# Kernel tuning notes

Hardware: AMD Instinct MI355X
Metric: run time of the kernel (lower is better)

## Reference

```python
import jax, jax.numpy as jnp
import numpy as np

B, S, M = 8, 2048, 256
D = 512          # input/memory feature dim
P = 512          # proj_dim
H = 8            # num_heads


def setup_inputs() -> dict:
    key = jax.random.key(0)
    ks = jax.random.split(key, 10)
    sc = 0.02
    return {
        "input_seq": jax.random.normal(ks[0], (B, S, D), jnp.float32),
        "memory_cells": jax.random.normal(ks[1], (B, M, D), jnp.float32),
        "Wk": jax.random.normal(ks[2], (D, P), jnp.float32) * sc,
        "bk": jnp.zeros((P,), jnp.float32),
        "Wv": jax.random.normal(ks[3], (D, P), jnp.float32) * sc,
        "bv": jnp.zeros((P,), jnp.float32),
        "Wq": jax.random.normal(ks[4], (H, D, P), jnp.float32) * sc,  # stacked per-head query Dense
        "bq": jnp.zeros((H, P), jnp.float32),
        "Wo": jax.random.normal(ks[5], (H * P, P), jnp.float32) * sc,
        "bo": jnp.zeros((P,), jnp.float32),
    }


def reference(input_seq, memory_cells, Wk, bk, Wv, bv, Wq, bq, Wo, bo):
    # shared key/value projections (multi-query: one K/V for all heads)
    ik = input_seq @ Wk + bk          # [B,S,P]
    mk = memory_cells @ Wk + bk       # [B,M,P]
    iv = input_seq @ Wv + bv          # [B,S,P]
    mv = memory_cells @ Wv + bv       # [B,M,P]

    # per-head queries from memory cells, all heads at once
    q = jnp.einsum('bmd,hdp->bhmp', memory_cells, Wq) + bq[None, :, None, :]  # [B,H,M,P]

    input_score = jnp.einsum('bhmp,bsp->bhms', q, ik)          # [B,H,M,S]
    self_score = jnp.sum(q * mk[:, None], axis=-1, keepdims=True)  # [B,H,M,1]
    score = jnp.concatenate([self_score, input_score], axis=-1)    # [B,H,M,S+1]
    score = score / jnp.sqrt(jnp.float32(P))
    attn = jax.nn.softmax(score, axis=-1)

    self_attn = attn[..., 0:1]                                  # [B,H,M,1]
    input_attn = attn[..., 1:]                                  # [B,H,M,S]
    val = jnp.einsum('bhms,bsp->bhmp', input_attn, iv) + self_attn * mv[:, None]

    # concat heads: [B,M,H*P]
    concat = jnp.transpose(val, (0, 2, 1, 3)).reshape(B, M, H * P)
    return concat @ Wo + bo           # [B,M,P]
```

## Files before the change

### kernel.cpp

```cpp
#include <hip/hip_runtime.h>

#define B_ 8
#define S_ 2048
#define M_ 256
#define D_ 512
#define P_ 512
#define H_ 8

#define SCALE 0.044194173824159216f

typedef __attribute__((ext_vector_type(8))) short bf16x8;
typedef __attribute__((ext_vector_type(4))) float f32x4;

static __device__ __forceinline__ float bf2f(short u) {
  union { float f; unsigned int i; } x;
  x.i = ((unsigned int)(unsigned short)u) << 16;
  return x.f;
}
static __device__ __forceinline__ short f2bf(float f) {
  union { float f; unsigned int i; } x;
  x.f = f;
  unsigned int r = (x.i + 0x7FFFu + ((x.i >> 16) & 1u)) >> 16;
  return (short)r;
}

static __device__ __forceinline__ void gll16(const short* g, short* l) {
  __builtin_amdgcn_global_load_lds(
      (const __attribute__((address_space(1))) void*)g,
      (__attribute__((address_space(3))) void*)l, 16, 0, 0);
}

#define LGKM_WAIT() asm volatile("s_waitcnt lgkmcnt(0)" ::: "memory")

__global__ __launch_bounds__(256) void cast_both(
    const float* __restrict__ inA, short* __restrict__ outA, int n4A,
    const float* __restrict__ inM, short* __restrict__ outM)
{
  int idx = blockIdx.x * 256 + threadIdx.x;
  const float* in = inA;
  short* out = outA;
  if (idx >= n4A) { idx -= n4A; in = inM; out = outM; }
  float4 v = ((const float4*)in)[idx];
  short o0 = f2bf(v.x), o1 = f2bf(v.y), o2 = f2bf(v.z), o3 = f2bf(v.w);
  uint2 pk;
  pk.x = (unsigned int)(unsigned short)o0 | ((unsigned int)(unsigned short)o1 << 16);
  pk.y = (unsigned int)(unsigned short)o2 | ((unsigned int)(unsigned short)o3 << 16);
  ((uint2*)out)[idx] = pk;
}

__global__ __launch_bounds__(256) void wtrans_g(
    const float* __restrict__ in, short* __restrict__ out, int kdim, int ndim)
{
  __shared__ float tile[32][33];
  const int t = threadIdx.x, tx = t & 31, ty = t >> 5;
  const size_t zofs = (size_t)blockIdx.z * kdim * ndim;
  const int n0 = blockIdx.x * 32, k0 = blockIdx.y * 32;
  const float* inp = in + zofs;
  short* outp = out + zofs;
#pragma unroll
  for (int i = 0; i < 4; ++i)
    tile[ty + 8 * i][tx] = inp[(size_t)(k0 + ty + 8 * i) * ndim + n0 + tx];
  __syncthreads();
#pragma unroll
  for (int i = 0; i < 4; ++i)
    outp[(size_t)(n0 + ty + 8 * i) * kdim + k0 + tx] = f2bf(tile[tx][ty + 8 * i]);
}

__global__ __launch_bounds__(256) void zero_f(float* __restrict__ p) {
  ((float4*)p)[blockIdx.x * 256 + threadIdx.x] = make_float4(0.f, 0.f, 0.f, 0.f);
}

template<int MODE, int K, int N, int LDA, int LDB>
__global__ __launch_bounds__(256) void gemm128(
    const short* __restrict__ Abase, const short* __restrict__ Bbase,
    const float* __restrict__ bias, void* __restrict__ Cv,
    const size_t aZ, const int bzsh, const size_t bZ, const size_t cZ,
    float* __restrict__ Ls,
    const float* __restrict__ eselfp, const short* __restrict__ mvbp)
{
  __shared__ short As[8192];
  __shared__ short Bs[8192];
  const int t = threadIdx.x;
  const int w = t >> 6, lane = t & 63, qd = lane >> 4, ln = lane & 15;
  const int z = blockIdx.z;
  const int n0 = blockIdx.x * 128, m0 = blockIdx.y * 128;
  const int wm = (w & 1) * 64, wn = (w >> 1) * 64;

  const short* A  = Abase + (size_t)z * aZ;
  const short* Bp = Bbase + (size_t)(z >> bzsh) * bZ;

  const int rr = t >> 3, gph = t & 7;
  const int gl = gph ^ ((rr >> 1) & 7);
  const short* gaT = A + (size_t)(m0 + rr) * LDA + gl * 8;
  const short* gbT = Bp + (size_t)(n0 + rr) * LDB + gl * 8;

  int aoff[4], boff[4];
#pragma unroll
  for (int mt = 0; mt < 4; ++mt) {
    int r = wm + mt * 16 + ln;
    aoff[mt] = r * 64 + (qd ^ ((r >> 1) & 7)) * 8;
  }
#pragma unroll
  for (int nt = 0; nt < 4; ++nt) {
    int r = wn + nt * 16 + ln;
    boff[nt] = r * 64 + (qd ^ ((r >> 1) & 7)) * 8;
  }

  f32x4 acc[4][4];
#pragma unroll
  for (int mt = 0; mt < 4; ++mt)
#pragma unroll
    for (int nt = 0; nt < 4; ++nt) acc[mt][nt] = (f32x4){0.f, 0.f, 0.f, 0.f};

  for (int kc = 0; kc < K; kc += 64) {
    __syncthreads();
#pragma unroll
    for (int c = 0; c < 4; ++c) {
      gll16(gaT + (size_t)c * 32 * LDA + kc, &As[c * 2048 + w * 512]);
      gll16(gbT + (size_t)c * 32 * LDB + kc, &Bs[c * 2048 + w * 512]);
    }
    __syncthreads();
#pragma unroll
    for (int ch = 0; ch < 2; ++ch) {
      const int x = ch * 32;
      bf16x8 af[4], bfr[4];
#pragma unroll
      for (int mt = 0; mt < 4; ++mt) af[mt] = *(const bf16x8*)&As[aoff[mt] ^ x];
#pragma unroll
      for (int nt = 0; nt < 4; ++nt) bfr[nt] = *(const bf16x8*)&Bs[boff[nt] ^ x];
#pragma unroll
      for (int mt = 0; mt < 4; ++mt)
#pragma unroll
        for (int nt = 0; nt < 4; ++nt)
          acc[mt][nt] = __builtin_amdgcn_mfma_f32_16x16x32_bf16(af[mt], bfr[nt], acc[mt][nt], 0, 0, 0);
    }
  }

  if constexpr (MODE == 5) {
#pragma unroll
    for (int nt = 0; nt < 4; ++nt) {
      const int col = n0 + wn + nt * 16 + ln;
#pragma unroll
      for (int mt = 0; mt < 4; ++mt)
#pragma unroll
        for (int r = 0; r < 4; ++r) {
          const int row = m0 + wm + mt * 16 + qd * 4 + r;
          ((float*)Cv)[(size_t)z * cZ + (size_t)row * N + col] = acc[mt][nt][r];
        }
    }
  } else if constexpr (MODE == 2) {
#pragma unroll
    for (int mt = 0; mt < 4; ++mt)
#pragma unroll
      for (int nt = 0; nt < 4; ++nt)
#pragma unroll
        for (int r = 0; r < 4; ++r)
          acc[mt][nt][r] = __expf(acc[mt][nt][r] * SCALE);
#pragma unroll
    for (int mt = 0; mt < 4; ++mt)
#pragma unroll
      for (int r = 0; r < 4; ++r) {
        float rsum = acc[mt][0][r] + acc[mt][1][r] + acc[mt][2][r] + acc[mt][3][r];
        rsum += __shfl_xor(rsum, 1);
        rsum += __shfl_xor(rsum, 2);
        rsum += __shfl_xor(rsum, 4);
        rsum += __shfl_xor(rsum, 8);
        if (ln == 0) {
          const int row = m0 + wm + mt * 16 + qd * 4 + r;
          atomicAdd(&Ls[(size_t)z * M_ + row], rsum);
        }
      }
#pragma unroll
    for (int nt = 0; nt < 4; ++nt) {
      const int col = n0 + wn + nt * 16 + ln;
#pragma unroll
      for (int mt = 0; mt < 4; ++mt)
#pragma unroll
        for (int r = 0; r < 4; ++r) {
          const int row = m0 + wm + mt * 16 + qd * 4 + r;
          ((short*)Cv)[(size_t)z * cZ + (size_t)row * N + col] = f2bf(acc[mt][nt][r]);
        }
    }
  } else if constexpr (MODE == 3) {
    const int zb = z >> 3, hh = z & 7;
#pragma unroll
    for (int mt = 0; mt < 4; ++mt)
#pragma unroll
      for (int r = 0; r < 4; ++r) {
        const int row = m0 + wm + mt * 16 + qd * 4 + r;
        const float es = eselfp[(size_t)z * M_ + row];
        const float inv = 1.f / (es + Ls[(size_t)z * M_ + row]);
        const short* mvr = mvbp + ((size_t)(zb * M_ + row)) * P_;
        short* outr = (short*)Cv + ((size_t)(zb * M_ + row)) * (H_ * P_) + (size_t)hh * P_;
#pragma unroll
        for (int nt = 0; nt < 4; ++nt) {
          const int col = n0 + wn + nt * 16 + ln;
          outr[col] = f2bf((acc[mt][nt][r] + es * bf2f(mvr[col])) * inv);
        }
      }
  } else {
#pragma unroll
    for (int nt = 0; nt < 4; ++nt) {
      const int col = n0 + wn + nt * 16 + ln;
      const float bc = bias[512 * z + col];
#pragma unroll
      for (int mt = 0; mt < 4; ++mt)
#pragma unroll
        for (int r = 0; r < 4; ++r) {
          const int row = m0 + wm + mt * 16 + qd * 4 + r;
          const int bidx = row >> 8, ml = row & 255;
          ((short*)Cv)[((size_t)(bidx * H_ + z) * M_ + ml) * N + col] = f2bf(acc[mt][nt][r] + bc);
        }
    }
  }
}

template<bool TRANSV>
__global__ __launch_bounds__(256) void proj_kv(
    const short* __restrict__ A,
    const short* __restrict__ WkT, const short* __restrict__ WvT,
    const float* __restrict__ bk, const float* __restrict__ bv,
    short* __restrict__ Ck, short* __restrict__ Cvv)
{
  __shared__ short As[8192];
  __shared__ short Bks[4096];
  __shared__ short Bvs[4096];
  const int t = threadIdx.x;
  const int w = t >> 6, lane = t & 63, qd = lane >> 4, ln = lane & 15;
  const int n0 = blockIdx.x * 64, m0 = blockIdx.y * 128;
  const int wm = (w & 1) * 64, wn2 = (w >> 1) * 32;

  const int rr = t >> 3, gph = t & 7;
  const int gl = gph ^ ((rr >> 1) & 7);
  const short* gaT = A + (size_t)(m0 + rr) * 512 + gl * 8;
  const short* gbkT = WkT + (size_t)(n0 + rr) * 512 + gl * 8;
  const short* gbvT = WvT + (size_t)(n0 + rr) * 512 + gl * 8;

  int aoff[4], boff[2];
#pragma unroll
  for (int mt = 0; mt < 4; ++mt) {
    int r = wm + mt * 16 + ln;
    aoff[mt] = r * 64 + (qd ^ ((r >> 1) & 7)) * 8;
  }
#pragma unroll
  for (int nt = 0; nt < 2; ++nt) {
    int r = wn2 + nt * 16 + ln;
    boff[nt] = r * 64 + (qd ^ ((r >> 1) & 7)) * 8;
  }

  f32x4 accK[4][2], accV[4][2];
#pragma unroll
  for (int mt = 0; mt < 4; ++mt)
#pragma unroll
    for (int nt = 0; nt < 2; ++nt) {
      accK[mt][nt] = (f32x4){0.f, 0.f, 0.f, 0.f};
      accV[mt][nt] = (f32x4){0.f, 0.f, 0.f, 0.f};
    }

  for (int kc = 0; kc < 512; kc += 64) {
    __syncthreads();
#pragma unroll
    for (int c = 0; c < 4; ++c)
      gll16(gaT + (size_t)c * 32 * 512 + kc, &As[c * 2048 + w * 512]);
#pragma unroll
    for (int c = 0; c < 2; ++c) {
      gll16(gbkT + (size_t)c * 32 * 512 + kc, &Bks[c * 2048 + w * 512]);
      gll16(gbvT + (size_t)c * 32 * 512 + kc, &Bvs[c * 2048 + w * 512]);
    }
    __syncthreads();
#pragma unroll
    for (int ch = 0; ch < 2; ++ch) {
      const int x = ch * 32;
      bf16x8 af[4], bkf[2], bvf[2];
#pragma unroll
      for (int mt = 0; mt < 4; ++mt) af[mt] = *(const bf16x8*)&As[aoff[mt] ^ x];
#pragma unroll
      for (int nt = 0; nt < 2; ++nt) {
        bkf[nt] = *(const bf16x8*)&Bks[boff[nt] ^ x];
        bvf[nt] = *(const bf16x8*)&Bvs[boff[nt] ^ x];
      }
#pragma unroll
      for (int mt = 0; mt < 4; ++mt)
#pragma unroll
        for (int nt = 0; nt < 2; ++nt) {
          accK[mt][nt] = __builtin_amdgcn_mfma_f32_16x16x32_bf16(af[mt], bkf[nt], accK[mt][nt], 0, 0, 0);
          accV[mt][nt] = __builtin_amdgcn_mfma_f32_16x16x32_bf16(af[mt], bvf[nt], accV[mt][nt], 0, 0, 0);
        }
    }
  }

#pragma unroll
  for (int nt = 0; nt < 2; ++nt) {
    const int col = n0 + wn2 + nt * 16 + ln;
    const float bc = bk[col];
#pragma unroll
    for (int mt = 0; mt < 4; ++mt)
#pragma unroll
      for (int r = 0; r < 4; ++r) {
        const int row = m0 + wm + mt * 16 + qd * 4 + r;
        Ck[(size_t)row * 512 + col] = f2bf(accK[mt][nt][r] + bc);
      }
  }

  if constexpr (!TRANSV) {
#pragma unroll
    for (int nt = 0; nt < 2; ++nt) {
      const int col = n0 + wn2 + nt * 16 + ln;
      const float bc = bv[col];
#pragma unroll
      for (int mt = 0; mt < 4; ++mt)
#pragma unroll
        for (int r = 0; r < 4; ++r) {
          const int row = m0 + wm + mt * 16 + qd * 4 + r;
          Cvv[(size_t)row * 512 + col] = f2bf(accV[mt][nt][r] + bc);
        }
    }
  } else {
    __syncthreads();
    short* ep = &As[w * 1280];
    const int lr = lane >> 1, lc16 = (lane & 1) * 16;
#pragma unroll
    for (int pass = 0; pass < 2; ++pass) {
#pragma unroll
      for (int mh = 0; mh < 2; ++mh) {
        const int mt = pass * 2 + mh;
#pragma unroll
        for (int nt = 0; nt < 2; ++nt) {
          const float bc = bv[n0 + wn2 + nt * 16 + ln];
#pragma unroll
          for (int r = 0; r < 4; ++r)
            ep[(nt * 16 + ln) * 40 + mh * 16 + qd * 4 + r] = f2bf(accV[mt][nt][r] + bc);
        }
      }
      LGKM_WAIT();
      const int srow0 = m0 + wm + pass * 32;
      const int bidx = srow0 >> 11;
      const int sloc = (srow0 & 2047) + lc16;
      const int pcol = n0 + wn2 + lr;
      short* outp = Cvv + (size_t)bidx * P_ * S_ + (size_t)pcol * S_ + sloc;
      *(bf16x8*)outp = *(const bf16x8*)&ep[lr * 40 + lc16];
      *(bf16x8*)(outp + 8) = *(const bf16x8*)&ep[lr * 40 + lc16 + 8];
      LGKM_WAIT();
    }
  }
}

__global__ __launch_bounds__(256) void reduce_wo(
    const float* __restrict__ partial, const float* __restrict__ bo,
    float* __restrict__ out)
{
  const int idx4 = blockIdx.x * 256 + threadIdx.x;
  float4 s = ((const float4*)bo)[idx4 & 127];
#pragma unroll
  for (int zz = 0; zz < 4; ++zz) {
    float4 p = ((const float4*)partial)[(size_t)zz * 262144 + idx4];
    s.x += p.x; s.y += p.y; s.z += p.z; s.w += p.w;
  }
  ((float4*)out)[idx4] = s;
}

__global__ __launch_bounds__(256) void selfscore(
    const short* __restrict__ qb, const short* __restrict__ mkb,
    float* __restrict__ eself)
{
  const int z = blockIdx.x, t = threadIdx.x;
  const short* qr = qb + ((size_t)z * M_ + t) * P_;
  const short* mr = mkb + ((size_t)(z >> 3) * M_ + t) * P_;
  float s = 0.f;
#pragma unroll 8
  for (int c = 0; c < P_; c += 8) {
    bf16x8 qv = *(const bf16x8*)(qr + c);
    bf16x8 mv = *(const bf16x8*)(mr + c);
#pragma unroll
    for (int j = 0; j < 8; ++j) s += bf2f(qv[j]) * bf2f(mv[j]);
  }
  eself[(size_t)z * M_ + t] = __expf(s * SCALE);
}

extern "C" void kernel_launch(void* const* d_in, const int* in_sizes, int n_in,
                              void* d_out, int out_size, void* d_ws, size_t ws_size,
                              hipStream_t stream) {
  const float* input_seq = (const float*)d_in[0];
  const float* memcells  = (const float*)d_in[1];
  const float* Wk = (const float*)d_in[2];
  const float* bk = (const float*)d_in[3];
  const float* Wv = (const float*)d_in[4];
  const float* bv = (const float*)d_in[5];
  const float* Wq = (const float*)d_in[6];
  const float* bq = (const float*)d_in[7];
  const float* Wo = (const float*)d_in[8];
  const float* bo = (const float*)d_in[9];
  float* out = (float*)d_out;

  short* ws = (short*)d_ws;
  size_t o = 0;
  short* valb = ws + o; o += (size_t)B_ * M_ * H_ * P_;
  short* WoT  = ws + o; o += (size_t)(H_ * P_) * P_;
  short* mvb  = ws + o; o += (size_t)B_ * M_ * P_;
  short* mkb  = ws + o; o += (size_t)B_ * M_ * P_;
  short* qb   = ws + o; o += (size_t)B_ * H_ * M_ * P_;
  short* ivT  = ws + o; o += (size_t)B_ * P_ * S_;
  short* ikb  = ws + o; o += (size_t)B_ * S_ * P_;
  float* partial = (float*)(ws + o); o += (size_t)B_ * H_ * M_ * P_;
  float* eself = (float*)(ws + o); o += 2 * (size_t)B_ * H_ * M_;
  float* Ls    = (float*)(ws + o); o += 2 * (size_t)B_ * H_ * M_;
  short* region2 = ws + o;
  short* Ab  = region2;
  short* Mb  = Ab + (size_t)B_ * S_ * D_;
  short* WkT = Mb + (size_t)B_ * M_ * D_;
  short* WvT = WkT + (size_t)D_ * P_;
  short* WqT = WvT + (size_t)D_ * P_;
  short* Eb  = region2;

  dim3 blk(256);

  const int n4A = B_ * S_ * D_ / 4;
  const int n4M = B_ * M_ * D_ / 4;
  cast_both<<<dim3((n4A + n4M) / 256), blk, 0, stream>>>(input_seq, Ab, n4A, memcells, Mb);
  wtrans_g<<<dim3(16, 16, 1), blk, 0, stream>>>(Wk, WkT, 512, 512);
  wtrans_g<<<dim3(16, 16, 1), blk, 0, stream>>>(Wv, WvT, 512, 512);
  wtrans_g<<<dim3(16, 16, 8), blk, 0, stream>>>(Wq, WqT, 512, 512);
  wtrans_g<<<dim3(16, 128, 1), blk, 0, stream>>>(Wo, WoT, 4096, 512);

  proj_kv<true><<<dim3(8, 128), blk, 0, stream>>>(Ab, WkT, WvT, bk, bv, ikb, ivT);
  proj_kv<false><<<dim3(8, 16), blk, 0, stream>>>(Mb, WkT, WvT, bk, bv, mkb, mvb);

  gemm128<1, 512, 512, 512, 512><<<dim3(4, 16, 8), blk, 0, stream>>>(
      Mb, WqT, bq, qb, 0, 0, (size_t)D_ * P_, 0, nullptr, nullptr, nullptr);

  zero_f<<<dim3(16), blk, 0, stream>>>(Ls);
  gemm128<2, 512, 2048, 512, 512><<<dim3(16, 2, 64), blk, 0, stream>>>(
      qb, ikb, nullptr, Eb, (size_t)M_ * P_, 3, (size_t)S_ * P_,
      (size_t)M_ * S_, Ls, nullptr, nullptr);

  selfscore<<<dim3(64), blk, 0, stream>>>(qb, mkb, eself);

  gemm128<3, 2048, 512, 2048, 2048><<<dim3(4, 2, 64), blk, 0, stream>>>(
      Eb, ivT, nullptr, valb, (size_t)M_ * S_, 3, (size_t)P_ * S_,
      0, Ls, eself, mvb);

  gemm128<5, 1024, 512, 4096, 4096><<<dim3(4, 16, 4), blk, 0, stream>>>(
      valb, WoT, nullptr, partial, 1024, 0, 1024,
      (size_t)2048 * 512, nullptr, nullptr, nullptr);
  reduce_wo<<<dim3(1024), blk, 0, stream>>>(partial, bo, out);
}
```

Baseline: 325.6 us.

## Double-buffer LDS tiles with K=32 steps in GEMM and KV projection

Both the generic GEMM and the fused K/V projection kernel move from a single 64-wide K tile, loaded and consumed between two barriers, to two 32-wide K tiles in LDS used as a double buffer. The next tile's global-to-LDS load is issued after the current fragments are read, so memory traffic overlaps with the MFMA work, and each iteration needs one barrier instead of two. The XOR swizzle and offsets change to match 32-element rows. In exchange there are twice as many iterations, each with less MFMA work to hide the load latency behind. There is also a vmcnt(0) wait every step, and correctness depends on the LDS buffer indexing staying consistent.

```diff
diff --git a/kernel.cpp b/kernel.cpp
--- a/kernel.cpp
+++ b/kernel.cpp
@@ -31,6 +31,8 @@
 }
 
 #define LGKM_WAIT() asm volatile("s_waitcnt lgkmcnt(0)" ::: "memory")
+#define VM_WAIT0() asm volatile("s_waitcnt vmcnt(0)" ::: "memory")
+#define SCHED_FENCE() asm volatile("" ::: "memory")
 
 __global__ __launch_bounds__(256) void cast_both(
     const float* __restrict__ inA, short* __restrict__ outA, int n4A,
@@ -89,21 +91,24 @@
   const short* A  = Abase + (size_t)z * aZ;
   const short* Bp = Bbase + (size_t)(z >> bzsh) * bZ;
 
-  const int rr = t >> 3, gph = t & 7;
-  const int gl = gph ^ ((rr >> 1) & 7);
-  const short* gaT = A + (size_t)(m0 + rr) * LDA + gl * 8;
-  const short* gbT = Bp + (size_t)(n0 + rr) * LDB + gl * 8;
+  const int rr = t >> 2, g0 = t & 3;
+  const int gs0 = g0 ^ ((rr >> 1) & 3);
+  const int gs1 = g0 ^ (((rr + 64) >> 1) & 3);
+  const short* ga0 = A + (size_t)(m0 + rr) * LDA + gs0 * 8;
+  const short* ga1 = A + (size_t)(m0 + rr + 64) * LDA + gs1 * 8;
+  const short* gb0 = Bp + (size_t)(n0 + rr) * LDB + gs0 * 8;
+  const short* gb1 = Bp + (size_t)(n0 + rr + 64) * LDB + gs1 * 8;
 
   int aoff[4], boff[4];
 #pragma unroll
   for (int mt = 0; mt < 4; ++mt) {
     int r = wm + mt * 16 + ln;
-    aoff[mt] = r * 64 + (qd ^ ((r >> 1) & 7)) * 8;
+    aoff[mt] = r * 32 + (qd ^ ((r >> 1) & 3)) * 8;
   }
 #pragma unroll
   for (int nt = 0; nt < 4; ++nt) {
     int r = wn + nt * 16 + ln;
-    boff[nt] = r * 64 + (qd ^ ((r >> 1) & 7)) * 8;
+    boff[nt] = r * 32 + (qd ^ ((r >> 1) & 3)) * 8;
   }
 
   f32x4 acc[4][4];
@@ -112,28 +117,35 @@
 #pragma unroll
     for (int nt = 0; nt < 4; ++nt) acc[mt][nt] = (f32x4){0.f, 0.f, 0.f, 0.f};
 
-  for (int kc = 0; kc < K; kc += 64) {
+  constexpr int NIT = K / 32;
+  gll16(ga0, &As[w * 512]);
+  gll16(ga1, &As[2048 + w * 512]);
+  gll16(gb0, &Bs[w * 512]);
+  gll16(gb1, &Bs[2048 + w * 512]);
+
+  for (int k = 0; k < NIT; ++k) {
+    VM_WAIT0();
     __syncthreads();
-#pragma unroll
-    for (int c = 0; c < 4; ++c) {
-      gll16(gaT + (size_t)c * 32 * LDA + kc, &As[c * 2048 + w * 512]);
-      gll16(gbT + (size_t)c * 32 * LDB + kc, &Bs[c * 2048 + w * 512]);
-    }
-    __syncthreads();
-#pragma unroll
-    for (int ch = 0; ch < 2; ++ch) {
-      const int x = ch * 32;
-      bf16x8 af[4], bfr[4];
-#pragma unroll
-      for (int mt = 0; mt < 4; ++mt) af[mt] = *(const bf16x8*)&As[aoff[mt] ^ x];
-#pragma unroll
-      for (int nt = 0; nt < 4; ++nt) bfr[nt] = *(const bf16x8*)&Bs[boff[nt] ^ x];
-#pragma unroll
-      for (int mt = 0; mt < 4; ++mt)
-#pragma unroll
-        for (int nt = 0; nt < 4; ++nt)
-          acc[mt][nt] = __builtin_amdgcn_mfma_f32_16x16x32_bf16(af[mt], bfr[nt], acc[mt][nt], 0, 0, 0);
-    }
+    const int cb = (k & 1) * 4096;
+    bf16x8 af[4], bfr[4];
+#pragma unroll
+    for (int mt = 0; mt < 4; ++mt) af[mt] = *(const bf16x8*)&As[cb + aoff[mt]];
+#pragma unroll
+    for (int nt = 0; nt < 4; ++nt) bfr[nt] = *(const bf16x8*)&Bs[cb + boff[nt]];
+    SCHED_FENCE();
+    if (k + 1 < NIT) {
+      const int kc = (k + 1) * 32;
+      const int nb = ((k + 1) & 1) * 4096;
+      gll16(ga0 + kc, &As[nb + w * 512]);
+      gll16(ga1 + kc, &As[nb + 2048 + w * 512]);
+      gll16(gb0 + kc, &Bs[nb + w * 512]);
+      gll16(gb1 + kc, &Bs[nb + 2048 + w * 512]);
+    }
+#pragma unroll
+    for (int mt = 0; mt < 4; ++mt)
+#pragma unroll
+      for (int nt = 0; nt < 4; ++nt)
+        acc[mt][nt] = __builtin_amdgcn_mfma_f32_16x16x32_bf16(af[mt], bfr[nt], acc[mt][nt], 0, 0, 0);
   }
 
   if constexpr (MODE == 5) {
@@ -230,22 +242,24 @@
   const int n0 = blockIdx.x * 64, m0 = blockIdx.y * 128;
   const int wm = (w & 1) * 64, wn2 = (w >> 1) * 32;
 
-  const int rr = t >> 3, gph = t & 7;
-  const int gl = gph ^ ((rr >> 1) & 7);
-  const short* gaT = A + (size_t)(m0 + rr) * 512 + gl * 8;
-  const short* gbkT = WkT + (size_t)(n0 + rr) * 512 + gl * 8;
-  const short* gbvT = WvT + (size_t)(n0 + rr) * 512 + gl * 8;
+  const int rr = t >> 2, g0 = t & 3;
+  const int gs0 = g0 ^ ((rr >> 1) & 3);
+  const int gs1 = g0 ^ (((rr + 64) >> 1) & 3);
+  const short* ga0 = A + (size_t)(m0 + rr) * 512 + gs0 * 8;
+  const short* ga1 = A + (size_t)(m0 + rr + 64) * 512 + gs1 * 8;
+  const short* gbk = WkT + (size_t)(n0 + rr) * 512 + gs0 * 8;
+  const short* gbv = WvT + (size_t)(n0 + rr) * 512 + gs0 * 8;
 
   int aoff[4], boff[2];
 #pragma unroll
   for (int mt = 0; mt < 4; ++mt) {
     int r = wm + mt * 16 + ln;
-    aoff[mt] = r * 64 + (qd ^ ((r >> 1) & 7)) * 8;
+    aoff[mt] = r * 32 + (qd ^ ((r >> 1) & 3)) * 8;
   }
 #pragma unroll
   for (int nt = 0; nt < 2; ++nt) {
     int r = wn2 + nt * 16 + ln;
-    boff[nt] = r * 64 + (qd ^ ((r >> 1) & 7)) * 8;
+    boff[nt] = r * 32 + (qd ^ ((r >> 1) & 3)) * 8;
   }
 
   f32x4 accK[4][2], accV[4][2];
@@ -257,36 +271,39 @@
       accV[mt][nt] = (f32x4){0.f, 0.f, 0.f, 0.f};
     }
 
-  for (int kc = 0; kc < 512; kc += 64) {
+  gll16(ga0, &As[w * 512]);
+  gll16(ga1, &As[2048 + w * 512]);
+  gll16(gbk, &Bks[w * 512]);
+  gll16(gbv, &Bvs[w * 512]);
+
+  for (int k = 0; k < 16; ++k) {
+    VM_WAIT0();
     __syncthreads();
-#pragma unroll
-    for (int c = 0; c < 4; ++c)
-      gll16(gaT + (size_t)c * 32 * 512 + kc, &As[c * 2048 + w * 512]);
-#pragma unroll
-    for (int c = 0; c < 2; ++c) {
-      gll16(gbkT + (size_t)c * 32 * 512 + kc, &Bks[c * 2048 + w * 512]);
-      gll16(gbvT + (size_t)c * 32 * 512 + kc, &Bvs[c * 2048 + w * 512]);
-    }
-    __syncthreads();
-#pragma unroll
-    for (int ch = 0; ch < 2; ++ch) {
-      const int x = ch * 32;
-      bf16x8 af[4], bkf[2], bvf[2];
-#pragma unroll
-      for (int mt = 0; mt < 4; ++mt) af[mt] = *(const bf16x8*)&As[aoff[mt] ^ x];
+    const int ca = (k & 1) * 4096, cbk = (k & 1) * 2048;
+    bf16x8 af[4], bkf[2], bvf[2];
+#pragma unroll
+    for (int mt = 0; mt < 4; ++mt) af[mt] = *(const bf16x8*)&As[ca + aoff[mt]];
+#pragma unroll
+    for (int nt = 0; nt < 2; ++nt) {
+      bkf[nt] = *(const bf16x8*)&Bks[cbk + boff[nt]];
+      bvf[nt] = *(const bf16x8*)&Bvs[cbk + boff[nt]];
+    }
+    SCHED_FENCE();
+    if (k + 1 < 16) {
+      const int kc = (k + 1) * 32;
+      const int na = ((k + 1) & 1) * 4096, nb = ((k + 1) & 1) * 2048;
+      gll16(ga0 + kc, &As[na + w * 512]);
+      gll16(ga1 + kc, &As[na + 2048 + w * 512]);
+      gll16(gbk + kc, &Bks[nb + w * 512]);
+      gll16(gbv + kc, &Bvs[nb + w * 512]);
+    }
+#pragma unroll
+    for (int mt = 0; mt < 4; ++mt)
 #pragma unroll
       for (int nt = 0; nt < 2; ++nt) {
-        bkf[nt] = *(const bf16x8*)&Bks[boff[nt] ^ x];
-        bvf[nt] = *(const bf16x8*)&Bvs[boff[nt] ^ x];
+        accK[mt][nt] = __builtin_amdgcn_mfma_f32_16x16x32_bf16(af[mt], bkf[nt], accK[mt][nt], 0, 0, 0);
+        accV[mt][nt] = __builtin_amdgcn_mfma_f32_16x16x32_bf16(af[mt], bvf[nt], accV[mt][nt], 0, 0, 0);
       }
-#pragma unroll
-      for (int mt = 0; mt < 4; ++mt)
-#pragma unroll
-        for (int nt = 0; nt < 2; ++nt) {
-          accK[mt][nt] = __builtin_amdgcn_mfma_f32_16x16x32_bf16(af[mt], bkf[nt], accK[mt][nt], 0, 0, 0);
-          accV[mt][nt] = __builtin_amdgcn_mfma_f32_16x16x32_bf16(af[mt], bvf[nt], accV[mt][nt], 0, 0, 0);
-        }
-    }
   }
 
 #pragma unroll
```

Result: slower. 335.6 us (+3.1%).
